# Performance work log

Measured on AMD Instinct MI355X. Metric: run time of the kernel, lower is better.

The kernel has to match this reference:

```python
import jax, jax.numpy as jnp
import numpy as np

ALPHA = 0.2  # LeakyReLU negative slope
NEG_INF = -9e15

def setup_inputs() -> dict:
    key = jax.random.key(0)
    k1, k2, k3, k4 = jax.random.split(key, 4)
    N, F_in, F_out = 8192, 256, 64
    h = jax.random.normal(k1, (N, F_in), dtype=jnp.float32)
    adj = jax.random.randint(k2, (N, N), 0, 2, dtype=jnp.int32)
    # xavier_uniform with gain=1.414
    def xavier(k, shape, gain=1.414):
        fan_in, fan_out = shape[0], shape[1]
        limit = gain * np.sqrt(6.0 / (fan_in + fan_out))
        return jax.random.uniform(k, shape, jnp.float32, -limit, limit)
    W = xavier(k3, (F_in, F_out))
    a = xavier(k4, (2 * F_out, 1))
    return {"h": h, "adj": adj, "W": W, "a": a}

def reference(h, adj, W, a):
    # Wh: (N, F_out)
    Wh = h @ W
    F_out = Wh.shape[1]
    a1 = a[:F_out, 0]   # (F_out,)
    a2 = a[F_out:, 0]   # (F_out,)
    # e_ij = LeakyReLU(Wh_i . a1 + Wh_j . a2)  -- equivalent to a^T [Wh_i || Wh_j]
    e = jax.nn.leaky_relu((Wh @ a1)[:, None] + (Wh @ a2)[None, :], negative_slope=ALPHA)
    scores = jnp.where(adj > 0, e, NEG_INF)
    attention = jax.nn.softmax(scores, axis=1)  # (N, N)
    h_prime = attention @ Wh                    # (N, F_out)
    return jax.nn.elu(h_prime)  # concat=True path
```

## Files before the change

kernel.cpp:

```cpp
#include <hip/hip_runtime.h>
#include <hip/hip_bf16.h>

#define N 8192
#define FIN 256
#define FOUT 64
#define NSLICE 8
#define SLICE_J (N / NSLICE)
#define NEG_INF -9.0e15f
#define L2E 1.4426950408889634f

typedef __attribute__((ext_vector_type(8))) short short8;
typedef __attribute__((ext_vector_type(4))) float f32x4;

static __device__ __forceinline__ short f2bf(float v) {
    __hip_bfloat16 b = __float2bfloat16(v);
    return __builtin_bit_cast(short, b);
}
static __device__ __forceinline__ float bf2f(short s) {
    unsigned u = ((unsigned)(unsigned short)s) << 16;
    return __builtin_bit_cast(float, u);
}
static __device__ __forceinline__ float exp2fast(float x) {
    return __builtin_amdgcn_exp2f(x);
}

__global__ __launch_bounds__(256) void k_wh(const float* __restrict__ h,
                                            const float* __restrict__ W,
                                            const float* __restrict__ a,
                                            float* __restrict__ Wh,
                                            float* __restrict__ s1,
                                            float* __restrict__ s2) {
    int wave = threadIdx.x >> 6, lane = threadIdx.x & 63;
    int i = blockIdx.x * 4 + wave;
    const float* hrow = h + (size_t)i * FIN;
    float acc = 0.f;
#pragma unroll 8
    for (int k = 0; k < FIN; k += 4) {
        float4 hv = *(const float4*)(hrow + k);
        acc += hv.x * W[(k + 0) * FOUT + lane];
        acc += hv.y * W[(k + 1) * FOUT + lane];
        acc += hv.z * W[(k + 2) * FOUT + lane];
        acc += hv.w * W[(k + 3) * FOUT + lane];
    }
    Wh[(size_t)i * FOUT + lane] = acc;
    float v1 = acc * a[lane];
    float v2 = acc * a[FOUT + lane];
#pragma unroll
    for (int off = 32; off; off >>= 1) {
        v1 += __shfl_xor(v1, off);
        v2 += __shfl_xor(v2, off);
    }
    if (lane == 0) { s1[i] = v1 * L2E; s2[i] = v2 * L2E; }
}

__global__ __launch_bounds__(256) void k_max(const float* __restrict__ s2,
                                             float* __restrict__ maxs2) {
    int t = threadIdx.x;
    float m = NEG_INF;
    for (int i = t; i < N; i += 256) m = fmaxf(m, s2[i]);
#pragma unroll
    for (int off = 32; off; off >>= 1) m = fmaxf(m, __shfl_xor(m, off));
    __shared__ float red[4];
    if ((t & 63) == 0) red[t >> 6] = m;
    __syncthreads();
    if (t == 0) {
        float r = fmaxf(fmaxf(red[0], red[1]), fmaxf(red[2], red[3]));
        maxs2[0] = r;
    }
}

__global__ __launch_bounds__(256) void k_repack(const float* __restrict__ Wh,
                                                short* __restrict__ WhB) {
    int t = blockIdx.x * 256 + threadIdx.x;
    int lane = t & 63, ft = (t >> 6) & 3, jt = t >> 8;
    int g = lane >> 4, r = lane & 15;
    short8 w;
#pragma unroll
    for (int q = 0; q < 8; ++q) {
        float v = Wh[(size_t)(jt * 32 + g * 8 + q) * FOUT + ft * 16 + r];
        w[q] = f2bf(v);
    }
    *((short8*)WhB + t) = w;
}

__global__ __launch_bounds__(128) void k_flash(const int* __restrict__ adj,
                                               const short* __restrict__ WhB,
                                               const float* __restrict__ s1,
                                               const float* __restrict__ s2,
                                               const float* __restrict__ maxs2,
                                               float* __restrict__ pO,
                                               float* __restrict__ pl) {
    int rb = blockIdx.x / NSLICE, sl = blockIdx.x % NSLICE;
    int wave = threadIdx.x >> 6, lane = threadIdx.x & 63;
    int r = lane & 15, g = lane >> 4;
    int row = rb * 32 + wave * 16 + r;

    __shared__ __align__(16) float s2s[SLICE_J];
    for (int t = threadIdx.x; t < SLICE_J; t += 128) s2s[t] = s2[sl * SLICE_J + t];
    __syncthreads();

    float s1i = s1[row];
    float xm = s1i + maxs2[0];
    float Mp = fmaxf(xm, 0.2f * xm);

    float l = 0.f;
    f32x4 acc0 = {0.f, 0.f, 0.f, 0.f};
    f32x4 acc1 = {0.f, 0.f, 0.f, 0.f};
    f32x4 acc2 = {0.f, 0.f, 0.f, 0.f};
    f32x4 acc3 = {0.f, 0.f, 0.f, 0.f};

    const int* arow = adj + (size_t)row * N + sl * SLICE_J + g * 8;

#pragma unroll 2
    for (int step = 0; step < SLICE_J / 32; ++step) {
        int4 av0 = *(const int4*)(arow + step * 32);
        int4 av1 = *(const int4*)(arow + step * 32 + 4);
        float4 sv0 = *(const float4*)&s2s[step * 32 + g * 8];
        float4 sv1 = *(const float4*)&s2s[step * 32 + g * 8 + 4];

        short8 af;
        auto pc = [&](int aval, float s2v) -> short {
            float x = s1i + s2v;
            float lr = fmaxf(x, 0.2f * x);
            float p = exp2fast(lr - Mp);
            p = aval > 0 ? p : 0.f;
            return f2bf(p);
        };
        af[0] = pc(av0.x, sv0.x); af[1] = pc(av0.y, sv0.y);
        af[2] = pc(av0.z, sv0.z); af[3] = pc(av0.w, sv0.w);
        af[4] = pc(av1.x, sv1.x); af[5] = pc(av1.y, sv1.y);
        af[6] = pc(av1.z, sv1.z); af[7] = pc(av1.w, sv1.w);

        l += bf2f(af[0]) + bf2f(af[1]) + bf2f(af[2]) + bf2f(af[3]) +
             bf2f(af[4]) + bf2f(af[5]) + bf2f(af[6]) + bf2f(af[7]);

        int jt = sl * (SLICE_J / 32) + step;
        const short8* bp = (const short8*)WhB + (size_t)jt * 256 + lane;
        acc0 = __builtin_amdgcn_mfma_f32_16x16x32_bf16(af, bp[0], acc0, 0, 0, 0);
        acc1 = __builtin_amdgcn_mfma_f32_16x16x32_bf16(af, bp[64], acc1, 0, 0, 0);
        acc2 = __builtin_amdgcn_mfma_f32_16x16x32_bf16(af, bp[128], acc2, 0, 0, 0);
        acc3 = __builtin_amdgcn_mfma_f32_16x16x32_bf16(af, bp[192], acc3, 0, 0, 0);
    }

    l += __shfl_xor(l, 16);
    l += __shfl_xor(l, 32);

    int base_row = rb * 32 + wave * 16;
    f32x4 accs[4] = {acc0, acc1, acc2, acc3};
#pragma unroll
    for (int nt = 0; nt < 4; ++nt) {
#pragma unroll
        for (int reg = 0; reg < 4; ++reg) {
            int orow = base_row + g * 4 + reg;
            pO[((size_t)orow * NSLICE + sl) * FOUT + nt * 16 + r] = accs[nt][reg];
        }
    }
    if (lane < 16) pl[(size_t)row * NSLICE + sl] = l;
}

__global__ __launch_bounds__(256) void k_merge(const float* __restrict__ pO,
                                               const float* __restrict__ pl,
                                               float* __restrict__ out) {
    int t = blockIdx.x * 256 + threadIdx.x;
    int row = t >> 6, f = t & 63;
    float L = 0.f, O = 0.f;
#pragma unroll
    for (int s = 0; s < NSLICE; ++s) {
        L += pl[(size_t)row * NSLICE + s];
        O += pO[((size_t)row * NSLICE + s) * FOUT + f];
    }
    float x = O / L;
    out[t] = x > 0.f ? x : expm1f(x);
}

extern "C" void kernel_launch(void* const* d_in, const int* in_sizes, int n_in,
                              void* d_out, int out_size, void* d_ws, size_t ws_size,
                              hipStream_t stream) {
    const float* h   = (const float*)d_in[0];
    const int*   adj = (const int*)d_in[1];
    const float* W   = (const float*)d_in[2];
    const float* a   = (const float*)d_in[3];
    float* out = (float*)d_out;

    char* ws = (char*)d_ws;
    float* Wh    = (float*)ws;
    short* WhB   = (short*)(ws + (2u << 20));
    float* s1    = (float*)(ws + (3u << 20));
    float* s2    = (float*)(ws + (3u << 20) + 32768);
    float* maxs2 = (float*)(ws + (3u << 20) + 65536);
    float* pO    = (float*)(ws + (4u << 20));
    float* pl    = (float*)(ws + (20u << 20));

    k_wh<<<N / 4, 256, 0, stream>>>(h, W, a, Wh, s1, s2);
    k_max<<<1, 256, 0, stream>>>(s2, maxs2);
    k_repack<<<(N / 32) * 4 * 64 / 256, 256, 0, stream>>>(Wh, WhB);
    k_flash<<<(N / 32) * NSLICE, 128, 0, stream>>>(adj, WhB, s1, s2, maxs2, pO, pl);
    k_merge<<<N * FOUT / 256, 256, 0, stream>>>(pO, pl, out);
}
```

Baseline: 122.0 us.

## Preload adjacency tile as ballot bitmasks with coalesced row loads in flash kernel

Before the main loop, each wave reads its 16 adjacency rows for the slice with fully coalesced 64-lane loads and compresses them into 64-bit ballot masks. Each lane keeps the 16 masks for its own row in registers. The inner loop then takes its 8 mask bits per step from registers instead of issuing strided int4 loads, and the loop is fully unrolled. The aim is better coalescing of the dominant adjacency read stream. In exchange, the prologue is serial and latency-bound, indexes chunks dynamically (which may spill to scratch unless fully unrolled), and leaves no overlap between adj loading and compute.

Result: no change. 120.1 us (-1.5%).

```diff
diff --git a/kernel.cpp b/kernel.cpp
--- a/kernel.cpp
+++ b/kernel.cpp
@@ -99,6 +99,20 @@
     for (int t = threadIdx.x; t < SLICE_J; t += 128) s2s[t] = s2[sl * SLICE_J + t];
     __syncthreads();
 
+    unsigned long long chunks[16];
+    {
+        int rbase = rb * 32 + wave * 16;
+        const int* abase = adj + (size_t)rbase * N + sl * SLICE_J;
+        for (int i = 0; i < 16; ++i) {
+            const int* ar = abase + (size_t)i * N;
+#pragma unroll
+            for (int w = 0; w < 16; ++w) {
+                unsigned long long bal = __ballot(ar[w * 64 + lane] > 0);
+                if (r == i) chunks[w] = bal;
+            }
+        }
+    }
+
     float s1i = s1[row];
     float xm = s1i + maxs2[0];
     float Mp = fmaxf(xm, 0.2f * xm);
@@ -109,27 +123,24 @@
     f32x4 acc2 = {0.f, 0.f, 0.f, 0.f};
     f32x4 acc3 = {0.f, 0.f, 0.f, 0.f};
 
-    const int* arow = adj + (size_t)row * N + sl * SLICE_J + g * 8;
-
-#pragma unroll 2
+#pragma unroll
     for (int step = 0; step < SLICE_J / 32; ++step) {
-        int4 av0 = *(const int4*)(arow + step * 32);
-        int4 av1 = *(const int4*)(arow + step * 32 + 4);
+        unsigned bits = (unsigned)((chunks[step >> 1] >>
+                                    (((step & 1) << 5) + (g << 3))) & 0xffull);
         float4 sv0 = *(const float4*)&s2s[step * 32 + g * 8];
         float4 sv1 = *(const float4*)&s2s[step * 32 + g * 8 + 4];
 
         short8 af;
-        auto pc = [&](int aval, float s2v) -> short {
+        auto pc = [&](unsigned bit, float s2v) -> short {
             float x = s1i + s2v;
             float lr = fmaxf(x, 0.2f * x);
             float p = exp2fast(lr - Mp);
-            p = aval > 0 ? p : 0.f;
-            return f2bf(p);
+            return bit ? f2bf(p) : (short)0;
         };
-        af[0] = pc(av0.x, sv0.x); af[1] = pc(av0.y, sv0.y);
-        af[2] = pc(av0.z, sv0.z); af[3] = pc(av0.w, sv0.w);
-        af[4] = pc(av1.x, sv1.x); af[5] = pc(av1.y, sv1.y);
-        af[6] = pc(av1.z, sv1.z); af[7] = pc(av1.w, sv1.w);
+        af[0] = pc(bits & 1u, sv0.x);        af[1] = pc((bits >> 1) & 1u, sv0.y);
+        af[2] = pc((bits >> 2) & 1u, sv0.z); af[3] = pc((bits >> 3) & 1u, sv0.w);
+        af[4] = pc((bits >> 4) & 1u, sv1.x); af[5] = pc((bits >> 5) & 1u, sv1.y);
+        af[6] = pc((bits >> 6) & 1u, sv1.z); af[7] = pc((bits >> 7) & 1u, sv1.w);
 
         l += bf2f(af[0]) + bf2f(af[1]) + bf2f(af[2]) + bf2f(af[3]) +
              bf2f(af[4]) + bf2f(af[5]) + bf2f(af[6]) + bf2f(af[7]);
```
